# Performance work log

Measured on AMD Instinct MI355X. Metric: run time of the kernel, lower is better.

Reference implementation:

```python
import math
import jax, jax.numpy as jnp
import numpy as np

EPS = 1e-5
NUM_HEADER = 2


def pos_encoding(C, T, dtype):
    i = jnp.arange(C)
    exp = -((i - (i % 2)).astype(dtype) / C)
    freqs = jnp.power(jnp.asarray(10000.0, dtype), exp)[:, None]      # [C,1]
    phases = ((i % 2).astype(dtype) * (np.pi / 2))[:, None]           # [C,1]
    pos = jnp.arange(T, dtype=dtype)[None, :]                         # [1,T]
    return jnp.sin(pos * freqs + phases)                              # [C,T]


def layernorm2d(x, g, b):
    # LayerNorm over (C,T) jointly, per batch element (nn.LayerNorm([C, length]))
    mu = jnp.mean(x, axis=(1, 2), keepdims=True)
    var = jnp.mean((x - mu) ** 2, axis=(1, 2), keepdims=True)
    return (x - mu) * jax.lax.rsqrt(var + EPS) * g[None] + b[None]


def dsconv(x, dw_w, dw_b, pw_w, pw_b):
    # depthwise conv1d (groups=C, 'same' padding for odd k) + pointwise 1x1
    C = x.shape[1]
    k = dw_w.shape[-1]
    y = jax.lax.conv_general_dilated(
        x, dw_w[:, None, :], (1,), [(k // 2, k // 2)],
        dimension_numbers=('NCH', 'OIH', 'NCH'), feature_group_count=C)
    y = y + dw_b[None, :, None]
    y = jnp.einsum('bct,oc->bot', y, pw_w) + pw_b[None, :, None]
    return y


def attention(x, mask, Wq, Wk, Wv, Wo):
    # Faithful to source bug: all heads use Wqs[1]/Wks[1]/Wvs[1] -> identical heads.
    xt = jnp.transpose(x, (0, 2, 1))          # [B,T,C]
    C = xt.shape[-1]
    dk = C / NUM_HEADER
    q = xt @ Wq                               # [B,T,dk]
    k_ = xt @ Wk
    v = xt @ Wv
    s = jnp.einsum('bqd,bkd->bqk', q, k_) * (1.0 / math.sqrt(dk))
    hmask = mask[:, None, :]                  # mask over keys
    s = s * hmask + (1 - hmask) * (-1e30)
    a = jax.nn.softmax(s, axis=2) * mask[:, :, None]
    head = a @ v                              # [B,T,dk]
    heads = jnp.tile(head, (1, 1, NUM_HEADER))  # concat of identical heads
    out = heads @ Wo                          # [B,T,C]
    return jnp.transpose(out, (0, 2, 1))      # [B,C,T]


def setup_inputs() -> dict:
    key = jax.random.key(0)
    B, C, T = 16, 128, 1024
    NCONV, K = 4, 7
    dk = C // NUM_HEADER
    ks = jax.random.split(key, 12)
    inp = {
        'x': jax.random.normal(ks[0], (B, C, T), jnp.float32),
        'mask': jnp.ones((B, T), jnp.float32),
        'dw_w': jax.random.normal(ks[1], (NCONV, C, K), jnp.float32) * math.sqrt(2.0 / K),
        'dw_b': jnp.zeros((NCONV, C), jnp.float32),
        'pw_w': jax.random.normal(ks[2], (NCONV, C, C), jnp.float32) * math.sqrt(2.0 / C),
        'pw_b': jnp.zeros((NCONV, C), jnp.float32),
        'norm0_g': jnp.ones((C, T), jnp.float32),
        'norm0_b': jnp.zeros((C, T), jnp.float32),
        'norms_g': jnp.ones((NCONV, C, T), jnp.float32),
        'norms_b': jnp.zeros((NCONV, C, T), jnp.float32),
        'norme_g': jnp.ones((C, T), jnp.float32),
        'norme_b': jnp.zeros((C, T), jnp.float32),
        'Wq': jax.random.normal(ks[3], (C, dk), jnp.float32) * math.sqrt(2.0 / (C + dk)),
        'Wk': jax.random.normal(ks[4], (C, dk), jnp.float32) * math.sqrt(2.0 / (C + dk)),
        'Wv': jax.random.normal(ks[5], (C, dk), jnp.float32) * math.sqrt(2.0 / (C + dk)),
        'Wo': jax.random.normal(ks[6], (C, C), jnp.float32) * math.sqrt(2.0 / C),
        'fc_w': jax.random.normal(ks[7], (C, C), jnp.float32) * (0.1 * math.sqrt(6.0 / (2 * C))),
        'fc_b': jnp.zeros((C,), jnp.float32),
    }
    return inp


def reference(x, mask, dw_w, dw_b, pw_w, pw_b, norm0_g, norm0_b,
              norms_g, norms_b, norme_g, norme_b,
              Wq, Wk, Wv, Wo, fc_w, fc_b):
    B, C, T = x.shape
    nconv = dw_w.shape[0]
    # dropout is identity in eval mode (reference is deterministic)
    out = x + pos_encoding(C, T, x.dtype)[None]
    res = layernorm2d(out, norm0_g, norm0_b)
    for i in range(nconv):
        out = dsconv(out, dw_w[i], dw_b[i], pw_w[i], pw_b[i])
        out = jax.nn.relu(out)
        out = out + res
        res = out
        out = layernorm2d(out, norms_g[i], norms_b[i])
    out = attention(out, mask, Wq, Wk, Wv, Wo)
    out = out + res
    res = out
    out = layernorm2d(out, norme_g, norme_b)
    out = jnp.einsum('bct,oc->bot', out, fc_w) + fc_b[None, :, None]
    out = jax.nn.relu(out)
    out = out + res
    return out
```

## Files before the change

### kernel.cpp

```cpp
#include <hip/hip_runtime.h>
#include <math.h>

#define BB 16
#define CC 128
#define TT 1024
#define KK 7
#define DK 64
#define NSPLIT 4

typedef float f32x4 __attribute__((ext_vector_type(4)));
typedef short s16x8 __attribute__((ext_vector_type(8)));

__device__ inline short f2bf(float f) {
  union { float f; unsigned u; } v; v.f = f;
  unsigned r = (v.u + 0x7FFFu + ((v.u >> 16) & 1u)) >> 16;
  return (short)r;
}

__device__ inline float bf2f(short s) {
  union { unsigned u; float f; } v;
  v.u = ((unsigned)(unsigned short)s) << 16;
  return v.f;
}

__device__ inline void block_partial_256(float s, float ss, float* dst) {
#pragma unroll
  for (int off = 32; off; off >>= 1) { s += __shfl_xor(s, off); ss += __shfl_xor(ss, off); }
  __shared__ float red[8];
  int w = threadIdx.x >> 6;
  if ((threadIdx.x & 63) == 0) { red[2 * w] = s; red[2 * w + 1] = ss; }
  __syncthreads();
  if (threadIdx.x == 0) {
    for (int i = 1; i < 4; ++i) { s += red[2 * i]; ss += red[2 * i + 1]; }
    dst[0] = s; dst[1] = ss;
  }
}

__device__ inline void ln_stats_from_parts(const float* part_batch, int n, float* sh) {
  if (threadIdx.x < 64) {
    float s = 0.f, ss = 0.f;
    for (int i = threadIdx.x; i < n; i += 64) { s += part_batch[2 * i]; ss += part_batch[2 * i + 1]; }
#pragma unroll
    for (int off = 32; off; off >>= 1) { s += __shfl_xor(s, off); ss += __shfl_xor(ss, off); }
    if (threadIdx.x == 0) {
      const float invN = 1.f / (float)(CC * TT);
      float mu = s * invN;
      sh[0] = mu;
      sh[1] = rsqrtf(ss * invN - mu * mu + 1e-5f);
    }
  }
  __syncthreads();
}

__global__ __launch_bounds__(256) void k_prep0(const float* __restrict__ pww,
                                               const float* __restrict__ Wq,
                                               const float* __restrict__ Wk,
                                               const float* __restrict__ Wv,
                                               const float* __restrict__ Wo,
                                               const float* __restrict__ fcw,
                                               const float* __restrict__ x,
                                               short* __restrict__ pwwb,
                                               short* __restrict__ wqkvb,
                                               short* __restrict__ wo2b,
                                               short* __restrict__ fcwb,
                                               float* __restrict__ part0) {
  if (blockIdx.x < 448) {
    int i = blockIdx.x * 256 + threadIdx.x;
    if (i < 65536) { pwwb[i] = f2bf(pww[i]); return; }
    i -= 65536;
    if (i < 24576) {
      int m = i >> 7, c = i & 127;
      int sel = m >> 6, d = m & 63;
      const float* srcp = sel == 0 ? Wq : (sel == 1 ? Wk : Wv);
      wqkvb[i] = f2bf(srcp[c * DK + d]);
      return;
    }
    i -= 24576;
    if (i < 8192) {
      int o = i >> 6, d = i & 63;
      wo2b[i] = f2bf(Wo[d * CC + o] + Wo[(d + 64) * CC + o]);
      return;
    }
    i -= 8192;
    fcwb[i] = f2bf(fcw[i]);
    return;
  }
  int w = threadIdx.x >> 6, lane = threadIdx.x & 63;
  int bc = (blockIdx.x - 448) * 4 + w;
  int c = bc & (CC - 1);
  float freq = expf(-((float)(c & ~1) * (1.f / (float)CC)) * 9.210340371976184f);
  float ph = (c & 1) ? 1.5707963267948966f : 0.f;
  const float* xr = x + (size_t)bc * TT;
  float s = 0.f, ss = 0.f;
#pragma unroll
  for (int k = 0; k < 4; ++k) {
    int t = (k * 64 + lane) * 4;
    float4 v = *(const float4*)(xr + t);
    v.x += sinf((float)(t + 0) * freq + ph);
    v.y += sinf((float)(t + 1) * freq + ph);
    v.z += sinf((float)(t + 2) * freq + ph);
    v.w += sinf((float)(t + 3) * freq + ph);
    s += v.x + v.y + v.z + v.w;
    ss += v.x * v.x + v.y * v.y + v.z * v.z + v.w * v.w;
  }
#pragma unroll
  for (int off = 32; off; off >>= 1) { s += __shfl_xor(s, off); ss += __shfl_xor(ss, off); }
  if (lane == 0) { part0[(size_t)bc * 2] = s; part0[(size_t)bc * 2 + 1] = ss; }
}

template <bool LN_IN, bool LN_RES, bool ADD_POS>
__global__ __launch_bounds__(256) void k_dsconv(const float* __restrict__ in,
                                                const float* __restrict__ lng,
                                                const float* __restrict__ lnb,
                                                const float* __restrict__ part_in, int npart,
                                                const float* __restrict__ dww,
                                                const float* __restrict__ dwb,
                                                const short* __restrict__ pwwb,
                                                const float* __restrict__ pwb,
                                                float* __restrict__ out,
                                                float* __restrict__ part_out) {
  int tile = blockIdx.x & 31, b = blockIdx.x >> 5;
  int t0 = tile * 32;
  __shared__ float stats[2];
  __shared__ float xs[CC][41];
  __shared__ float xr2[CC][33];
  __shared__ __align__(16) short Dt[32][136];
  ln_stats_from_parts(part_in + (size_t)b * npart * 2, npart, stats);
  float mu = stats[0], rs = stats[1];

  for (int i = threadIdx.x; i < CC * 10; i += 256) {
    int c = i / 10, q = i - c * 10;
    int tb = t0 - 4 + q * 4;
    const float* rowp = in + ((size_t)b * CC + c) * TT;
    float freq = 0.f, ph = 0.f;
    if (ADD_POS) {
      freq = expf(-((float)(c & ~1) * (1.f / (float)CC)) * 9.210340371976184f);
      ph = (c & 1) ? 1.5707963267948966f : 0.f;
    }
    float r0, r1, r2, r3, o0, o1, o2, o3;
    bool full = (tb >= 0) && (tb + 4 <= TT);
    if (full) {
      float4 v = *(const float4*)(rowp + tb);
      if (ADD_POS) {
        v.x += sinf((float)(tb + 0) * freq + ph);
        v.y += sinf((float)(tb + 1) * freq + ph);
        v.z += sinf((float)(tb + 2) * freq + ph);
        v.w += sinf((float)(tb + 3) * freq + ph);
      }
      r0 = v.x; r1 = v.y; r2 = v.z; r3 = v.w;
      o0 = r0; o1 = r1; o2 = r2; o3 = r3;
      if (LN_IN) {
        float4 g = *(const float4*)(lng + (size_t)c * TT + tb);
        float4 bv = *(const float4*)(lnb + (size_t)c * TT + tb);
        o0 = (r0 - mu) * rs * g.x + bv.x;
        o1 = (r1 - mu) * rs * g.y + bv.y;
        o2 = (r2 - mu) * rs * g.z + bv.z;
        o3 = (r3 - mu) * rs * g.w + bv.w;
      }
    } else {
      float rr[4], oo[4];
#pragma unroll
      for (int k = 0; k < 4; ++k) {
        int t = tb + k;
        bool inb = (t >= 0) && (t < TT);
        float rv = 0.f;
        if (inb) {
          rv = rowp[t];
          if (ADD_POS) rv += sinf((float)t * freq + ph);
        }
        rr[k] = rv;
        float ov = rv;
        if (LN_IN && inb)
          ov = (rv - mu) * rs * lng[(size_t)c * TT + t] + lnb[(size_t)c * TT + t];
        oo[k] = ov;
      }
      r0 = rr[0]; r1 = rr[1]; r2 = rr[2]; r3 = rr[3];
      o0 = oo[0]; o1 = oo[1]; o2 = oo[2]; o3 = oo[3];
    }
    if (LN_IN && q >= 1 && q <= 8) {
      int tl = (q - 1) * 4;
      xr2[c][tl] = r0; xr2[c][tl + 1] = r1; xr2[c][tl + 2] = r2; xr2[c][tl + 3] = r3;
    }
    int base = q * 4;
    xs[c][base] = o0; xs[c][base + 1] = o1; xs[c][base + 2] = o2; xs[c][base + 3] = o3;
  }
  __syncthreads();
  for (int i = threadIdx.x; i < 32 * CC; i += 256) {
    int t = i >> 7, c = i & 127;
    float a = dwb[c];
#pragma unroll
    for (int j = 0; j < KK; ++j) a += dww[c * KK + j] * xs[c][t + j + 1];
    Dt[t][c] = f2bf(a);
  }
  __syncthreads();

  int w = threadIdx.x >> 6, lane = threadIdx.x & 63;
  int lo = lane & 15, hi = lane >> 4;
  f32x4 acc[2][2];
#pragma unroll
  for (int mt = 0; mt < 2; ++mt)
#pragma unroll
    for (int nt = 0; nt < 2; ++nt) { acc[mt][nt][0] = 0.f; acc[mt][nt][1] = 0.f; acc[mt][nt][2] = 0.f; acc[mt][nt][3] = 0.f; }
#pragma unroll
  for (int ks = 0; ks < 4; ++ks) {
    s16x8 b0 = *(const s16x8*)&Dt[lo][ks * 32 + hi * 8];
    s16x8 b1 = *(const s16x8*)&Dt[16 + lo][ks * 32 + hi * 8];
    s16x8 a0 = *(const s16x8*)&pwwb[(size_t)(w * 32 + lo) * CC + ks * 32 + hi * 8];
    s16x8 a1 = *(const s16x8*)&pwwb[(size_t)(w * 32 + 16 + lo) * CC + ks * 32 + hi * 8];
    acc[0][0] = __builtin_amdgcn_mfma_f32_16x16x32_bf16(a0, b0, acc[0][0], 0, 0, 0);
    acc[0][1] = __builtin_amdgcn_mfma_f32_16x16x32_bf16(a0, b1, acc[0][1], 0, 0, 0);
    acc[1][0] = __builtin_amdgcn_mfma_f32_16x16x32_bf16(a1, b0, acc[1][0], 0, 0, 0);
    acc[1][1] = __builtin_amdgcn_mfma_f32_16x16x32_bf16(a1, b1, acc[1][1], 0, 0, 0);
  }

  float s = 0.f, ss = 0.f;
#pragma unroll
  for (int mt = 0; mt < 2; ++mt)
#pragma unroll
    for (int nt = 0; nt < 2; ++nt)
#pragma unroll
      for (int r = 0; r < 4; ++r) {
        int row = w * 32 + mt * 16 + hi * 4 + r;
        int tl = nt * 16 + lo;
        int t = t0 + tl;
        float v = acc[mt][nt][r] + pwb[row];
        v = v > 0.f ? v : 0.f;
        float rv;
        if (LN_RES) {
          float raw = xs[row][tl + 4];
          rv = (raw - mu) * rs * lng[row * TT + t] + lnb[row * TT + t];
        } else if (LN_IN) {
          rv = xr2[row][tl];
        } else {
          rv = xs[row][tl + 4];
        }
        v += rv;
        xr2[row][tl] = v;
        s += v; ss += v * v;
      }
  __syncthreads();
  for (int u = threadIdx.x; u < 1024; u += 256) {
    int c = u >> 3, q = u & 7;
    float4 o4;
    o4.x = xr2[c][q * 4]; o4.y = xr2[c][q * 4 + 1];
    o4.z = xr2[c][q * 4 + 2]; o4.w = xr2[c][q * 4 + 3];
    *(float4*)(out + ((size_t)b * CC + c) * TT + t0 + q * 4) = o4;
  }
  block_partial_256(s, ss, part_out + (size_t)blockIdx.x * 2);
}

__global__ __launch_bounds__(256) void k_qkv(const float* __restrict__ in,
                                             const float* __restrict__ lng,
                                             const float* __restrict__ lnb,
                                             const float* __restrict__ part_in,
                                             const short* __restrict__ wqkvb,
                                             short* __restrict__ q,
                                             short* __restrict__ k,
                                             short* __restrict__ vt) {
  int tile = blockIdx.x & 31, b = blockIdx.x >> 5;
  int t0 = tile * 32;
  __shared__ float stats[2];
  __shared__ __align__(16) short Dt[32][136];
  __shared__ __align__(16) short stgQ[32 * 64];
  __shared__ __align__(16) short stgK[32 * 64];
  __shared__ __align__(16) short stgV[64][40];
  ln_stats_from_parts(part_in + (size_t)b * 64, 32, stats);
  float mu = stats[0], rs = stats[1];
  for (int i = threadIdx.x; i < CC * 8; i += 256) {
    int c = i >> 3, qq = i & 7;
    int t = qq * 4;
    size_t off = (size_t)c * TT + t0 + t;
    float4 v = *(const float4*)(in + (size_t)b * CC * TT + off);
    float4 g = *(const float4*)(lng + off);
    float4 bb = *(const float4*)(lnb + off);
    Dt[t + 0][c] = f2bf((v.x - mu) * rs * g.x + bb.x);
    Dt[t + 1][c] = f2bf((v.y - mu) * rs * g.y + bb.y);
    Dt[t + 2][c] = f2bf((v.z - mu) * rs * g.z + bb.z);
    Dt[t + 3][c] = f2bf((v.w - mu) * rs * g.w + bb.w);
  }
  __syncthreads();

  int w = threadIdx.x >> 6, lane = threadIdx.x & 63;
  int lo = lane & 15, hi = lane >> 4;
  f32x4 acc[3][2];
#pragma unroll
  for (int mt = 0; mt < 3; ++mt)
#pragma unroll
    for (int nt = 0; nt < 2; ++nt) { acc[mt][nt][0] = 0.f; acc[mt][nt][1] = 0.f; acc[mt][nt][2] = 0.f; acc[mt][nt][3] = 0.f; }
#pragma unroll
  for (int ks = 0; ks < 4; ++ks) {
    s16x8 b0 = *(const s16x8*)&Dt[lo][ks * 32 + hi * 8];
    s16x8 b1 = *(const s16x8*)&Dt[16 + lo][ks * 32 + hi * 8];
#pragma unroll
    for (int mt = 0; mt < 3; ++mt) {
      s16x8 a = *(const s16x8*)&wqkvb[(size_t)(w * 48 + mt * 16 + lo) * CC + ks * 32 + hi * 8];
      acc[mt][0] = __builtin_amdgcn_mfma_f32_16x16x32_bf16(a, b0, acc[mt][0], 0, 0, 0);
      acc[mt][1] = __builtin_amdgcn_mfma_f32_16x16x32_bf16(a, b1, acc[mt][1], 0, 0, 0);
    }
  }
#pragma unroll
  for (int mt = 0; mt < 3; ++mt)
#pragma unroll
    for (int nt = 0; nt < 2; ++nt) {
      int m0 = w * 48 + mt * 16 + hi * 4;
      int tl = nt * 16 + lo;
      short pv[4];
#pragma unroll
      for (int j = 0; j < 4; ++j) pv[j] = f2bf(acc[mt][nt][j]);
      if (m0 < 64) {
        *(short4*)&stgQ[tl * 64 + m0] = make_short4(pv[0], pv[1], pv[2], pv[3]);
      } else if (m0 < 128) {
        *(short4*)&stgK[tl * 64 + (m0 - 64)] = make_short4(pv[0], pv[1], pv[2], pv[3]);
      } else {
        int d = m0 - 128;
#pragma unroll
        for (int j = 0; j < 4; ++j) stgV[d + j][tl] = pv[j];
      }
    }
  __syncthreads();
  {
    int t = threadIdx.x >> 3, ch = threadIdx.x & 7;
    *(s16x8*)(q + ((size_t)b * TT + t0 + t) * DK + ch * 8) = *(const s16x8*)&stgQ[t * 64 + ch * 8];
    *(s16x8*)(k + ((size_t)b * TT + t0 + t) * DK + ch * 8) = *(const s16x8*)&stgK[t * 64 + ch * 8];
    int d = threadIdx.x >> 2, cv = threadIdx.x & 3;
    *(s16x8*)(vt + ((size_t)b * DK + d) * TT + t0 + cv * 8) = *(const s16x8*)&stgV[d][cv * 8];
  }
}

__global__ __launch_bounds__(128) void k_attn(const short* __restrict__ qb,
                                              const short* __restrict__ kbuf,
                                              const short* __restrict__ vtb,
                                              const float* __restrict__ mask,
                                              short* __restrict__ pacch,
                                              float* __restrict__ pml) {
  int sp = blockIdx.x & (NSPLIT - 1);
  int qt = (blockIdx.x >> 2) & 31;
  int b = blockIdx.x >> 7;
  int w = threadIdx.x >> 6, lane = threadIdx.x & 63;
  int lo = lane & 15, hi = lane >> 4;

  __shared__ __align__(16) short ks[64][72];
  __shared__ __align__(16) short vt[64][72];
  __shared__ __align__(16) short ps[2][16][68];
  __shared__ float ms[64];

  const short* qp = qb + ((size_t)b * TT + qt * 32 + w * 16 + lo) * DK + hi * 8;
  s16x8 aq0 = *(const s16x8*)qp;
  s16x8 aq1 = *(const s16x8*)(qp + 32);

  f32x4 acc[4];
  float m_i[4], l_i[4];
#pragma unroll
  for (int r = 0; r < 4; ++r) {
    m_i[r] = -3.0e38f; l_i[r] = 0.f;
#pragma unroll
    for (int nt = 0; nt < 4; ++nt) acc[nt][r] = 0.f;
  }
  const float scale = 0.125f;

  for (int kb2 = sp * (TT / 64 / NSPLIT); kb2 < (sp + 1) * (TT / 64 / NSPLIT); ++kb2) {
    __syncthreads();
    for (int i = threadIdx.x; i < 512; i += 128) {
      int r = i >> 3, ch = i & 7;
      *(s16x8*)&ks[r][ch * 8] =
          *(const s16x8*)(kbuf + ((size_t)b * TT + kb2 * 64 + r) * DK + ch * 8);
      *(s16x8*)&vt[r][ch * 8] =
          *(const s16x8*)(vtb + ((size_t)b * DK + r) * TT + kb2 * 64 + ch * 8);
    }
    if (threadIdx.x < 64) ms[threadIdx.x] = mask[(size_t)b * TT + kb2 * 64 + threadIdx.x];
    __syncthreads();

    f32x4 sc[4];
#pragma unroll
    for (int nt = 0; nt < 4; ++nt) {
      f32x4 z; z[0] = 0.f; z[1] = 0.f; z[2] = 0.f; z[3] = 0.f;
      s16x8 bk0 = *(const s16x8*)&ks[nt * 16 + lo][hi * 8];
      s16x8 bk1 = *(const s16x8*)&ks[nt * 16 + lo][32 + hi * 8];
      z = __builtin_amdgcn_mfma_f32_16x16x32_bf16(aq0, bk0, z, 0, 0, 0);
      z = __builtin_amdgcn_mfma_f32_16x16x32_bf16(aq1, bk1, z, 0, 0, 0);
      sc[nt] = z;
    }
#pragma unroll
    for (int nt = 0; nt < 4; ++nt) {
      float mv = ms[nt * 16 + lo];
      float addv = (1.f - mv) * -1e30f;
#pragma unroll
      for (int r = 0; r < 4; ++r) sc[nt][r] = sc[nt][r] * scale * mv + addv;
    }
    float alpha[4];
#pragma unroll
    for (int r = 0; r < 4; ++r) {
      float m0 = fmaxf(fmaxf(sc[0][r], sc[1][r]), fmaxf(sc[2][r], sc[3][r]));
#pragma unroll
      for (int off = 1; off < 16; off <<= 1) m0 = fmaxf(m0, __shfl_xor(m0, off));
      float mn = fmaxf(m_i[r], m0);
      alpha[r] = __expf(m_i[r] - mn);
      m_i[r] = mn;
    }
    float psum[4] = {0.f, 0.f, 0.f, 0.f};
#pragma unroll
    for (int nt = 0; nt < 4; ++nt)
#pragma unroll
      for (int r = 0; r < 4; ++r) {
        float p = __expf(sc[nt][r] - m_i[r]);
        psum[r] += p;
        ps[w][hi * 4 + r][nt * 16 + lo] = f2bf(p);
      }
#pragma unroll
    for (int r = 0; r < 4; ++r) {
      float sum = psum[r];
#pragma unroll
      for (int off = 1; off < 16; off <<= 1) sum += __shfl_xor(sum, off);
      l_i[r] = l_i[r] * alpha[r] + sum;
    }
#pragma unroll
    for (int nt = 0; nt < 4; ++nt)
#pragma unroll
      for (int r = 0; r < 4; ++r) acc[nt][r] *= alpha[r];

    s16x8 ap0 = *(const s16x8*)&ps[w][lo][hi * 8];
    s16x8 ap1 = *(const s16x8*)&ps[w][lo][32 + hi * 8];
#pragma unroll
    for (int nt = 0; nt < 4; ++nt) {
      s16x8 bv0 = *(const s16x8*)&vt[nt * 16 + lo][hi * 8];
      s16x8 bv1 = *(const s16x8*)&vt[nt * 16 + lo][32 + hi * 8];
      acc[nt] = __builtin_amdgcn_mfma_f32_16x16x32_bf16(ap0, bv0, acc[nt], 0, 0, 0);
      acc[nt] = __builtin_amdgcn_mfma_f32_16x16x32_bf16(ap1, bv1, acc[nt], 0, 0, 0);
    }
  }
  __syncthreads();
  short* pc = &ks[0][0];
#pragma unroll
  for (int r = 0; r < 4; ++r) {
    int row = w * 16 + hi * 4 + r;
#pragma unroll
    for (int nt = 0; nt < 4; ++nt) pc[row * 64 + nt * 16 + lo] = f2bf(acc[nt][r]);
    if (lo == 0) {
      size_t mb = (((size_t)b * TT + qt * 32 + row) * NSPLIT + sp) * 2;
      pml[mb] = m_i[r];
      pml[mb + 1] = l_i[r];
    }
  }
  __syncthreads();
  for (int u = threadIdx.x; u < 256; u += 128) {
    int row = u >> 3, ch = u & 7;
    size_t pb = (((size_t)b * TT + qt * 32 + row) * NSPLIT + sp) * DK;
    *(s16x8*)(pacch + pb + ch * 8) = *(const s16x8*)&pc[row * 64 + ch * 8];
  }
}

__global__ __launch_bounds__(256) void k_attnout2(const short* __restrict__ pacch,
                                                  const float* __restrict__ pml,
                                                  const float* __restrict__ mask,
                                                  const short* __restrict__ wo2b,
                                                  const float* __restrict__ res,
                                                  float* __restrict__ out,
                                                  float* __restrict__ part_out) {
  int tile = blockIdx.x & 31, b = blockIdx.x >> 5;
  int t0 = tile * 32;
  __shared__ __align__(16) short Ht[32][72];
  __shared__ float ot[128][33];
  {
    int i = threadIdx.x;
    int tr = i >> 3, q = i & 7;
    size_t rb = (size_t)b * TT + t0 + tr;
    float m[NSPLIT], l[NSPLIT];
#pragma unroll
    for (int s = 0; s < NSPLIT; ++s) {
      m[s] = pml[(rb * NSPLIT + s) * 2];
      l[s] = pml[(rb * NSPLIT + s) * 2 + 1];
    }
    float M = fmaxf(fmaxf(m[0], m[1]), fmaxf(m[2], m[3]));
    float wgt[NSPLIT], L = 0.f;
#pragma unroll
    for (int s = 0; s < NSPLIT; ++s) { wgt[s] = __expf(m[s] - M); L += wgt[s] * l[s]; }
    float inv = mask[rb] / L;
    float o[8] = {0.f, 0.f, 0.f, 0.f, 0.f, 0.f, 0.f, 0.f};
#pragma unroll
    for (int s = 0; s < NSPLIT; ++s) {
      s16x8 pv = *(const s16x8*)(pacch + (rb * NSPLIT + s) * DK + q * 8);
#pragma unroll
      for (int j = 0; j < 8; ++j) o[j] += wgt[s] * bf2f(pv[j]);
    }
    short h[8];
#pragma unroll
    for (int j = 0; j < 8; ++j) h[j] = f2bf(o[j] * inv);
    *(s16x8*)&Ht[tr][q * 8] = *(const s16x8*)h;
  }
  __syncthreads();

  int w = threadIdx.x >> 6, lane = threadIdx.x & 63;
  int lo = lane & 15, hi = lane >> 4;
  f32x4 acc[2][2];
#pragma unroll
  for (int mt = 0; mt < 2; ++mt)
#pragma unroll
    for (int nt = 0; nt < 2; ++nt) { acc[mt][nt][0] = 0.f; acc[mt][nt][1] = 0.f; acc[mt][nt][2] = 0.f; acc[mt][nt][3] = 0.f; }
#pragma unroll
  for (int ks = 0; ks < 2; ++ks) {
    s16x8 b0 = *(const s16x8*)&Ht[lo][ks * 32 + hi * 8];
    s16x8 b1 = *(const s16x8*)&Ht[16 + lo][ks * 32 + hi * 8];
    s16x8 a0 = *(const s16x8*)&wo2b[(size_t)(w * 32 + lo) * DK + ks * 32 + hi * 8];
    s16x8 a1 = *(const s16x8*)&wo2b[(size_t)(w * 32 + 16 + lo) * DK + ks * 32 + hi * 8];
    acc[0][0] = __builtin_amdgcn_mfma_f32_16x16x32_bf16(a0, b0, acc[0][0], 0, 0, 0);
    acc[0][1] = __builtin_amdgcn_mfma_f32_16x16x32_bf16(a0, b1, acc[0][1], 0, 0, 0);
    acc[1][0] = __builtin_amdgcn_mfma_f32_16x16x32_bf16(a1, b0, acc[1][0], 0, 0, 0);
    acc[1][1] = __builtin_amdgcn_mfma_f32_16x16x32_bf16(a1, b1, acc[1][1], 0, 0, 0);
  }
  float s = 0.f, ss = 0.f;
#pragma unroll
  for (int mt = 0; mt < 2; ++mt)
#pragma unroll
    for (int nt = 0; nt < 2; ++nt)
#pragma unroll
      for (int r = 0; r < 4; ++r) {
        int row = w * 32 + mt * 16 + hi * 4 + r;
        int tl = nt * 16 + lo;
        size_t idx = ((size_t)b * CC + row) * TT + t0 + tl;
        float v = acc[mt][nt][r] + res[idx];
        ot[row][tl] = v;
        s += v; ss += v * v;
      }
  __syncthreads();
  for (int u = threadIdx.x; u < 1024; u += 256) {
    int c = u >> 3, q = u & 7;
    float4 o4;
    o4.x = ot[c][q * 4]; o4.y = ot[c][q * 4 + 1];
    o4.z = ot[c][q * 4 + 2]; o4.w = ot[c][q * 4 + 3];
    *(float4*)(out + ((size_t)b * CC + c) * TT + t0 + q * 4) = o4;
  }
  block_partial_256(s, ss, part_out + (size_t)blockIdx.x * 2);
}

__global__ __launch_bounds__(256) void k_fc(const float* __restrict__ in,
                                            const float* __restrict__ lng,
                                            const float* __restrict__ lnb,
                                            const float* __restrict__ part_in,
                                            const short* __restrict__ fcwb,
                                            const float* __restrict__ fb,
                                            float* __restrict__ out) {
  int tile = blockIdx.x & 31, b = blockIdx.x >> 5;
  int t0 = tile * 32;
  __shared__ float stats[2];
  __shared__ float xr2[CC][33];
  __shared__ __align__(16) short Dt[32][136];
  ln_stats_from_parts(part_in + (size_t)b * 64, 32, stats);
  float mu = stats[0], rs = stats[1];
  for (int i = threadIdx.x; i < CC * 8; i += 256) {
    int c = i >> 3, q = i & 7;
    int t = q * 4;
    size_t off = (size_t)c * TT + t0 + t;
    float4 v = *(const float4*)(in + (size_t)b * CC * TT + off);
    float4 g = *(const float4*)(lng + off);
    float4 bb = *(const float4*)(lnb + off);
    xr2[c][t] = v.x; xr2[c][t + 1] = v.y; xr2[c][t + 2] = v.z; xr2[c][t + 3] = v.w;
    Dt[t + 0][c] = f2bf((v.x - mu) * rs * g.x + bb.x);
    Dt[t + 1][c] = f2bf((v.y - mu) * rs * g.y + bb.y);
    Dt[t + 2][c] = f2bf((v.z - mu) * rs * g.z + bb.z);
    Dt[t + 3][c] = f2bf((v.w - mu) * rs * g.w + bb.w);
  }
  __syncthreads();

  int w = threadIdx.x >> 6, lane = threadIdx.x & 63;
  int lo = lane & 15, hi = lane >> 4;
  f32x4 acc[2][2];
#pragma unroll
  for (int mt = 0; mt < 2; ++mt)
#pragma unroll
    for (int nt = 0; nt < 2; ++nt) { acc[mt][nt][0] = 0.f; acc[mt][nt][1] = 0.f; acc[mt][nt][2] = 0.f; acc[mt][nt][3] = 0.f; }
#pragma unroll
  for (int ks = 0; ks < 4; ++ks) {
    s16x8 b0 = *(const s16x8*)&Dt[lo][ks * 32 + hi * 8];
    s16x8 b1 = *(const s16x8*)&Dt[16 + lo][ks * 32 + hi * 8];
    s16x8 a0 = *(const s16x8*)&fcwb[(size_t)(w * 32 + lo) * CC + ks * 32 + hi * 8];
    s16x8 a1 = *(const s16x8*)&fcwb[(size_t)(w * 32 + 16 + lo) * CC + ks * 32 + hi * 8];
    acc[0][0] = __builtin_amdgcn_mfma_f32_16x16x32_bf16(a0, b0, acc[0][0], 0, 0, 0);
    acc[0][1] = __builtin_amdgcn_mfma_f32_16x16x32_bf16(a0, b1, acc[0][1], 0, 0, 0);
    acc[1][0] = __builtin_amdgcn_mfma_f32_16x16x32_bf16(a1, b0, acc[1][0], 0, 0, 0);
    acc[1][1] = __builtin_amdgcn_mfma_f32_16x16x32_bf16(a1, b1, acc[1][1], 0, 0, 0);
  }
#pragma unroll
  for (int mt = 0; mt < 2; ++mt)
#pragma unroll
    for (int nt = 0; nt < 2; ++nt)
#pragma unroll
      for (int r = 0; r < 4; ++r) {
        int row = w * 32 + mt * 16 + hi * 4 + r;
        int tl = nt * 16 + lo;
        float v = acc[mt][nt][r] + fb[row];
        v = v > 0.f ? v : 0.f;
        xr2[row][tl] = v + xr2[row][tl];
      }
  __syncthreads();
  for (int u = threadIdx.x; u < 1024; u += 256) {
    int c = u >> 3, q = u & 7;
    float4 o4;
    o4.x = xr2[c][q * 4]; o4.y = xr2[c][q * 4 + 1];
    o4.z = xr2[c][q * 4 + 2]; o4.w = xr2[c][q * 4 + 3];
    *(float4*)(out + ((size_t)b * CC + c) * TT + t0 + q * 4) = o4;
  }
}

extern "C" void kernel_launch(void* const* d_in, const int* in_sizes, int n_in,
                              void* d_out, int out_size, void* d_ws, size_t ws_size,
                              hipStream_t stream) {
  const float* x    = (const float*)d_in[0];
  const float* mask = (const float*)d_in[1];
  const float* dww  = (const float*)d_in[2];
  const float* dwb  = (const float*)d_in[3];
  const float* pww  = (const float*)d_in[4];
  const float* pwb  = (const float*)d_in[5];
  const float* n0g  = (const float*)d_in[6];
  const float* n0b  = (const float*)d_in[7];
  const float* nsg  = (const float*)d_in[8];
  const float* nsb  = (const float*)d_in[9];
  const float* neg_ = (const float*)d_in[10];
  const float* neb  = (const float*)d_in[11];
  const float* Wq   = (const float*)d_in[12];
  const float* Wk   = (const float*)d_in[13];
  const float* Wv   = (const float*)d_in[14];
  const float* Wo   = (const float*)d_in[15];
  const float* fcw  = (const float*)d_in[16];
  const float* fcb  = (const float*)d_in[17];
  float* out = (float*)d_out;

  float* W = (float*)d_ws;
  const size_t NBCT = (size_t)BB * CC * TT;
  const size_t NBTD = (size_t)BB * TT * DK;
  const size_t CT = (size_t)CC * TT;
  float* O     = W;
  float* S     = W + NBCT;
  float* PART0 = W + 2 * NBCT;
  float* PARTS = PART0 + 4096;
  float* PML   = PARTS + 5 * 1024;
  short* QB    = (short*)(PML + (size_t)BB * TT * NSPLIT * 2);
  short* KB    = QB + NBTD;
  short* VT    = KB + NBTD;
  short* PACCH = VT + NBTD;
  short* PWWB  = PACCH + NBTD * NSPLIT;
  short* WQKVB = PWWB + 65536;
  short* WO2B  = WQKVB + 24576;
  short* FCWB  = WO2B + 8192;

  k_prep0<<<960, 256, 0, stream>>>(pww, Wq, Wk, Wv, Wo, fcw, x,
                                   PWWB, WQKVB, WO2B, FCWB, PART0);
  k_dsconv<false, true, true><<<BB * 32, 256, 0, stream>>>(
      x, n0g, n0b, PART0, 128, dww, dwb, PWWB, pwb, S, PARTS);
  k_dsconv<true, false, false><<<BB * 32, 256, 0, stream>>>(
      S, nsg + 0 * CT, nsb + 0 * CT, PARTS, 32,
      dww + 1 * CC * KK, dwb + 1 * CC, PWWB + 1 * CC * CC, pwb + 1 * CC, O, PARTS + 1024);
  k_dsconv<true, false, false><<<BB * 32, 256, 0, stream>>>(
      O, nsg + 1 * CT, nsb + 1 * CT, PARTS + 1024, 32,
      dww + 2 * CC * KK, dwb + 2 * CC, PWWB + 2 * CC * CC, pwb + 2 * CC, S, PARTS + 2048);
  k_dsconv<true, false, false><<<BB * 32, 256, 0, stream>>>(
      S, nsg + 2 * CT, nsb + 2 * CT, PARTS + 2048, 32,
      dww + 3 * CC * KK, dwb + 3 * CC, PWWB + 3 * CC * CC, pwb + 3 * CC, O, PARTS + 3072);
  k_qkv<<<BB * 32, 256, 0, stream>>>(O, nsg + 3 * CT, nsb + 3 * CT, PARTS + 3072,
                                     WQKVB, QB, KB, VT);
  k_attn<<<BB * 32 * NSPLIT, 128, 0, stream>>>(QB, KB, VT, mask, PACCH, PML);
  k_attnout2<<<BB * 32, 256, 0, stream>>>(PACCH, PML, mask, WO2B, O, S, PARTS + 4096);
  k_fc<<<BB * 32, 256, 0, stream>>>(S, neg_, neb, PARTS + 4096, FCWB, fcb, out);
}
```

Baseline: 192.7 us.

## Fuse split-K flash attention with output projection in one kernel

Merges the split-K attention kernel and the combine/output-projection kernel into one 256-thread kernel. Each block handles a 32-query tile, and its two 128-thread halves process the two halves of the keys. They then combine their partial softmax state through shared memory before running the Wo projection, residual add and LN partial sums. This removes the global round trip of bf16 partial accumulators and m/l values and one kernel launch. In exchange the attention grid shrinks from 2048 to 512 blocks, and each half walks 8 key blocks serially instead of 4, which reduces parallelism.

```diff
diff --git a/kernel.cpp b/kernel.cpp
--- a/kernel.cpp
+++ b/kernel.cpp
@@ -6,7 +6,6 @@
 #define TT 1024
 #define KK 7
 #define DK 64
-#define NSPLIT 4
 
 typedef float f32x4 __attribute__((ext_vector_type(4)));
 typedef short s16x8 __attribute__((ext_vector_type(8)));
@@ -15,12 +14,6 @@
   union { float f; unsigned u; } v; v.f = f;
   unsigned r = (v.u + 0x7FFFu + ((v.u >> 16) & 1u)) >> 16;
   return (short)r;
-}
-
-__device__ inline float bf2f(short s) {
-  union { unsigned u; float f; } v;
-  v.u = ((unsigned)(unsigned short)s) << 16;
-  return v.f;
 }
 
 __device__ inline void block_partial_256(float s, float ss, float* dst) {
@@ -327,24 +320,39 @@
   }
 }
 
-__global__ __launch_bounds__(128) void k_attn(const short* __restrict__ qb,
-                                              const short* __restrict__ kbuf,
-                                              const short* __restrict__ vtb,
-                                              const float* __restrict__ mask,
-                                              short* __restrict__ pacch,
-                                              float* __restrict__ pml) {
-  int sp = blockIdx.x & (NSPLIT - 1);
-  int qt = (blockIdx.x >> 2) & 31;
-  int b = blockIdx.x >> 7;
-  int w = threadIdx.x >> 6, lane = threadIdx.x & 63;
-  int lo = lane & 15, hi = lane >> 4;
-
-  __shared__ __align__(16) short ks[64][72];
-  __shared__ __align__(16) short vt[64][72];
-  __shared__ __align__(16) short ps[2][16][68];
-  __shared__ float ms[64];
-
-  const short* qp = qb + ((size_t)b * TT + qt * 32 + w * 16 + lo) * DK + hi * 8;
+struct AtHalf {
+  short ks[64][72];
+  short vt[64][72];
+  short ps[2][16][68];
+  float ms[64];
+};
+union AtShared {
+  AtHalf h[2];
+  float ot[128 * 33];
+};
+
+__global__ __launch_bounds__(256) void k_attnfused(const short* __restrict__ qb,
+                                                   const short* __restrict__ kbuf,
+                                                   const short* __restrict__ vtb,
+                                                   const float* __restrict__ mask,
+                                                   const short* __restrict__ wo2b,
+                                                   const float* __restrict__ res,
+                                                   float* __restrict__ out,
+                                                   float* __restrict__ part_out) {
+  int tile = blockIdx.x & 31, b = blockIdx.x >> 5;
+  int t0 = tile * 32;
+  __shared__ AtShared U;
+  __shared__ __align__(16) short Ht[32][72];
+
+  const int tid = threadIdx.x;
+  const int half = tid >> 7;
+  const int ltid = tid & 127;
+  const int hw = ltid >> 6;
+  const int lane = ltid & 63;
+  const int lo = lane & 15, hi = lane >> 4;
+  AtHalf& A = U.h[half];
+
+  const short* qp = qb + ((size_t)b * TT + t0 + hw * 16 + lo) * DK + hi * 8;
   s16x8 aq0 = *(const s16x8*)qp;
   s16x8 aq1 = *(const s16x8*)(qp + 32);
 
@@ -358,31 +366,32 @@
   }
   const float scale = 0.125f;
 
-  for (int kb2 = sp * (TT / 64 / NSPLIT); kb2 < (sp + 1) * (TT / 64 / NSPLIT); ++kb2) {
+  for (int it2 = 0; it2 < 8; ++it2) {
+    int kb2 = half * 8 + it2;
     __syncthreads();
-    for (int i = threadIdx.x; i < 512; i += 128) {
+    for (int i = ltid; i < 512; i += 128) {
       int r = i >> 3, ch = i & 7;
-      *(s16x8*)&ks[r][ch * 8] =
+      *(s16x8*)&A.ks[r][ch * 8] =
           *(const s16x8*)(kbuf + ((size_t)b * TT + kb2 * 64 + r) * DK + ch * 8);
-      *(s16x8*)&vt[r][ch * 8] =
+      *(s16x8*)&A.vt[r][ch * 8] =
           *(const s16x8*)(vtb + ((size_t)b * DK + r) * TT + kb2 * 64 + ch * 8);
     }
-    if (threadIdx.x < 64) ms[threadIdx.x] = mask[(size_t)b * TT + kb2 * 64 + threadIdx.x];
+    if (ltid < 64) A.ms[ltid] = mask[(size_t)b * TT + kb2 * 64 + ltid];
     __syncthreads();
 
     f32x4 sc[4];
 #pragma unroll
     for (int nt = 0; nt < 4; ++nt) {
       f32x4 z; z[0] = 0.f; z[1] = 0.f; z[2] = 0.f; z[3] = 0.f;
-      s16x8 bk0 = *(const s16x8*)&ks[nt * 16 + lo][hi * 8];
-      s16x8 bk1 = *(const s16x8*)&ks[nt * 16 + lo][32 + hi * 8];
+      s16x8 bk0 = *(const s16x8*)&A.ks[nt * 16 + lo][hi * 8];
+      s16x8 bk1 = *(const s16x8*)&A.ks[nt * 16 + lo][32 + hi * 8];
       z = __builtin_amdgcn_mfma_f32_16x16x32_bf16(aq0, bk0, z, 0, 0, 0);
       z = __builtin_amdgcn_mfma_f32_16x16x32_bf16(aq1, bk1, z, 0, 0, 0);
       sc[nt] = z;
     }
 #pragma unroll
     for (int nt = 0; nt < 4; ++nt) {
-      float mv = ms[nt * 16 + lo];
+      float mv = A.ms[nt * 16 + lo];
       float addv = (1.f - mv) * -1e30f;
 #pragma unroll
       for (int r = 0; r < 4; ++r) sc[nt][r] = sc[nt][r] * scale * mv + addv;
@@ -404,7 +413,7 @@
       for (int r = 0; r < 4; ++r) {
         float p = __expf(sc[nt][r] - m_i[r]);
         psum[r] += p;
-        ps[w][hi * 4 + r][nt * 16 + lo] = f2bf(p);
+        A.ps[hw][hi * 4 + r][nt * 16 + lo] = f2bf(p);
       }
 #pragma unroll
     for (int r = 0; r < 4; ++r) {
@@ -418,95 +427,66 @@
 #pragma unroll
       for (int r = 0; r < 4; ++r) acc[nt][r] *= alpha[r];
 
-    s16x8 ap0 = *(const s16x8*)&ps[w][lo][hi * 8];
-    s16x8 ap1 = *(const s16x8*)&ps[w][lo][32 + hi * 8];
+    s16x8 ap0 = *(const s16x8*)&A.ps[hw][lo][hi * 8];
+    s16x8 ap1 = *(const s16x8*)&A.ps[hw][lo][32 + hi * 8];
 #pragma unroll
     for (int nt = 0; nt < 4; ++nt) {
-      s16x8 bv0 = *(const s16x8*)&vt[nt * 16 + lo][hi * 8];
-      s16x8 bv1 = *(const s16x8*)&vt[nt * 16 + lo][32 + hi * 8];
+      s16x8 bv0 = *(const s16x8*)&A.vt[nt * 16 + lo][hi * 8];
+      s16x8 bv1 = *(const s16x8*)&A.vt[nt * 16 + lo][32 + hi * 8];
       acc[nt] = __builtin_amdgcn_mfma_f32_16x16x32_bf16(ap0, bv0, acc[nt], 0, 0, 0);
       acc[nt] = __builtin_amdgcn_mfma_f32_16x16x32_bf16(ap1, bv1, acc[nt], 0, 0, 0);
     }
   }
   __syncthreads();
-  short* pc = &ks[0][0];
-#pragma unroll
-  for (int r = 0; r < 4; ++r) {
-    int row = w * 16 + hi * 4 + r;
-#pragma unroll
-    for (int nt = 0; nt < 4; ++nt) pc[row * 64 + nt * 16 + lo] = f2bf(acc[nt][r]);
-    if (lo == 0) {
-      size_t mb = (((size_t)b * TT + qt * 32 + row) * NSPLIT + sp) * 2;
-      pml[mb] = m_i[r];
-      pml[mb + 1] = l_i[r];
-    }
-  }
-  __syncthreads();
-  for (int u = threadIdx.x; u < 256; u += 128) {
-    int row = u >> 3, ch = u & 7;
-    size_t pb = (((size_t)b * TT + qt * 32 + row) * NSPLIT + sp) * DK;
-    *(s16x8*)(pacch + pb + ch * 8) = *(const s16x8*)&pc[row * 64 + ch * 8];
-  }
-}
-
-__global__ __launch_bounds__(256) void k_attnout2(const short* __restrict__ pacch,
-                                                  const float* __restrict__ pml,
-                                                  const float* __restrict__ mask,
-                                                  const short* __restrict__ wo2b,
-                                                  const float* __restrict__ res,
-                                                  float* __restrict__ out,
-                                                  float* __restrict__ part_out) {
-  int tile = blockIdx.x & 31, b = blockIdx.x >> 5;
-  int t0 = tile * 32;
-  __shared__ __align__(16) short Ht[32][72];
-  __shared__ float ot[128][33];
-  {
-    int i = threadIdx.x;
-    int tr = i >> 3, q = i & 7;
-    size_t rb = (size_t)b * TT + t0 + tr;
-    float m[NSPLIT], l[NSPLIT];
-#pragma unroll
-    for (int s = 0; s < NSPLIT; ++s) {
-      m[s] = pml[(rb * NSPLIT + s) * 2];
-      l[s] = pml[(rb * NSPLIT + s) * 2 + 1];
-    }
-    float M = fmaxf(fmaxf(m[0], m[1]), fmaxf(m[2], m[3]));
-    float wgt[NSPLIT], L = 0.f;
-#pragma unroll
-    for (int s = 0; s < NSPLIT; ++s) { wgt[s] = __expf(m[s] - M); L += wgt[s] * l[s]; }
-    float inv = mask[rb] / L;
-    float o[8] = {0.f, 0.f, 0.f, 0.f, 0.f, 0.f, 0.f, 0.f};
-#pragma unroll
-    for (int s = 0; s < NSPLIT; ++s) {
-      s16x8 pv = *(const s16x8*)(pacch + (rb * NSPLIT + s) * DK + q * 8);
-#pragma unroll
-      for (int j = 0; j < 8; ++j) o[j] += wgt[s] * bf2f(pv[j]);
-    }
-    short h[8];
-#pragma unroll
-    for (int j = 0; j < 8; ++j) h[j] = f2bf(o[j] * inv);
-    *(s16x8*)&Ht[tr][q * 8] = *(const s16x8*)h;
-  }
-  __syncthreads();
-
-  int w = threadIdx.x >> 6, lane = threadIdx.x & 63;
-  int lo = lane & 15, hi = lane >> 4;
-  f32x4 acc[2][2];
+  float* cmb = (float*)&U.h[0];
+  float* ml1 = (float*)&U.h[1];
+  if (half == 1) {
+#pragma unroll
+    for (int r = 0; r < 4; ++r) {
+      int row = hw * 16 + hi * 4 + r;
+#pragma unroll
+      for (int nt = 0; nt < 4; ++nt) cmb[row * 64 + nt * 16 + lo] = acc[nt][r];
+      if (lo == 0) { ml1[row * 2] = m_i[r]; ml1[row * 2 + 1] = l_i[r]; }
+    }
+  }
+  __syncthreads();
+  if (half == 0) {
+#pragma unroll
+    for (int r = 0; r < 4; ++r) {
+      int row = hw * 16 + hi * 4 + r;
+      float m1 = ml1[row * 2], l1 = ml1[row * 2 + 1];
+      float M = fmaxf(m_i[r], m1);
+      float w0 = __expf(m_i[r] - M), w1 = __expf(m1 - M);
+      float L = w0 * l_i[r] + w1 * l1;
+      float inv = mask[(size_t)b * TT + t0 + row] / L;
+#pragma unroll
+      for (int nt = 0; nt < 4; ++nt)
+        Ht[row][nt * 16 + lo] =
+            f2bf((w0 * acc[nt][r] + w1 * cmb[row * 64 + nt * 16 + lo]) * inv);
+    }
+  }
+  __syncthreads();
+  int w4 = tid >> 6;
+  int flane = tid & 63;
+  int flo = flane & 15, fhi = flane >> 4;
+  f32x4 acc2[2][2];
 #pragma unroll
   for (int mt = 0; mt < 2; ++mt)
 #pragma unroll
-    for (int nt = 0; nt < 2; ++nt) { acc[mt][nt][0] = 0.f; acc[mt][nt][1] = 0.f; acc[mt][nt][2] = 0.f; acc[mt][nt][3] = 0.f; }
+    for (int nt = 0; nt < 2; ++nt) { acc2[mt][nt][0] = 0.f; acc2[mt][nt][1] = 0.f; acc2[mt][nt][2] = 0.f; acc2[mt][nt][3] = 0.f; }
 #pragma unroll
   for (int ks = 0; ks < 2; ++ks) {
-    s16x8 b0 = *(const s16x8*)&Ht[lo][ks * 32 + hi * 8];
-    s16x8 b1 = *(const s16x8*)&Ht[16 + lo][ks * 32 + hi * 8];
-    s16x8 a0 = *(const s16x8*)&wo2b[(size_t)(w * 32 + lo) * DK + ks * 32 + hi * 8];
-    s16x8 a1 = *(const s16x8*)&wo2b[(size_t)(w * 32 + 16 + lo) * DK + ks * 32 + hi * 8];
-    acc[0][0] = __builtin_amdgcn_mfma_f32_16x16x32_bf16(a0, b0, acc[0][0], 0, 0, 0);
-    acc[0][1] = __builtin_amdgcn_mfma_f32_16x16x32_bf16(a0, b1, acc[0][1], 0, 0, 0);
-    acc[1][0] = __builtin_amdgcn_mfma_f32_16x16x32_bf16(a1, b0, acc[1][0], 0, 0, 0);
-    acc[1][1] = __builtin_amdgcn_mfma_f32_16x16x32_bf16(a1, b1, acc[1][1], 0, 0, 0);
-  }
+    s16x8 b0 = *(const s16x8*)&Ht[flo][ks * 32 + fhi * 8];
+    s16x8 b1 = *(const s16x8*)&Ht[16 + flo][ks * 32 + fhi * 8];
+    s16x8 a0 = *(const s16x8*)&wo2b[(size_t)(w4 * 32 + flo) * DK + ks * 32 + fhi * 8];
+    s16x8 a1 = *(const s16x8*)&wo2b[(size_t)(w4 * 32 + 16 + flo) * DK + ks * 32 + fhi * 8];
+    acc2[0][0] = __builtin_amdgcn_mfma_f32_16x16x32_bf16(a0, b0, acc2[0][0], 0, 0, 0);
+    acc2[0][1] = __builtin_amdgcn_mfma_f32_16x16x32_bf16(a0, b1, acc2[0][1], 0, 0, 0);
+    acc2[1][0] = __builtin_amdgcn_mfma_f32_16x16x32_bf16(a1, b0, acc2[1][0], 0, 0, 0);
+    acc2[1][1] = __builtin_amdgcn_mfma_f32_16x16x32_bf16(a1, b1, acc2[1][1], 0, 0, 0);
+  }
+  __syncthreads();
+  float* otp = U.ot;
   float s = 0.f, ss = 0.f;
 #pragma unroll
   for (int mt = 0; mt < 2; ++mt)
@@ -514,19 +494,19 @@
     for (int nt = 0; nt < 2; ++nt)
 #pragma unroll
       for (int r = 0; r < 4; ++r) {
-        int row = w * 32 + mt * 16 + hi * 4 + r;
-        int tl = nt * 16 + lo;
+        int row = w4 * 32 + mt * 16 + fhi * 4 + r;
+        int tl = nt * 16 + flo;
         size_t idx = ((size_t)b * CC + row) * TT + t0 + tl;
-        float v = acc[mt][nt][r] + res[idx];
-        ot[row][tl] = v;
+        float v = acc2[mt][nt][r] + res[idx];
+        otp[row * 33 + tl] = v;
         s += v; ss += v * v;
       }
   __syncthreads();
-  for (int u = threadIdx.x; u < 1024; u += 256) {
+  for (int u = tid; u < 1024; u += 256) {
     int c = u >> 3, q = u & 7;
     float4 o4;
-    o4.x = ot[c][q * 4]; o4.y = ot[c][q * 4 + 1];
-    o4.z = ot[c][q * 4 + 2]; o4.w = ot[c][q * 4 + 3];
+    o4.x = otp[c * 33 + q * 4]; o4.y = otp[c * 33 + q * 4 + 1];
+    o4.z = otp[c * 33 + q * 4 + 2]; o4.w = otp[c * 33 + q * 4 + 3];
     *(float4*)(out + ((size_t)b * CC + c) * TT + t0 + q * 4) = o4;
   }
   block_partial_256(s, ss, part_out + (size_t)blockIdx.x * 2);
@@ -632,12 +612,10 @@
   float* S     = W + NBCT;
   float* PART0 = W + 2 * NBCT;
   float* PARTS = PART0 + 4096;
-  float* PML   = PARTS + 5 * 1024;
-  short* QB    = (short*)(PML + (size_t)BB * TT * NSPLIT * 2);
+  short* QB    = (short*)(PARTS + 5 * 1024);
   short* KB    = QB + NBTD;
   short* VT    = KB + NBTD;
-  short* PACCH = VT + NBTD;
-  short* PWWB  = PACCH + NBTD * NSPLIT;
+  short* PWWB  = VT + NBTD;
   short* WQKVB = PWWB + 65536;
   short* WO2B  = WQKVB + 24576;
   short* FCWB  = WO2B + 8192;
@@ -657,7 +635,6 @@
       dww + 3 * CC * KK, dwb + 3 * CC, PWWB + 3 * CC * CC, pwb + 3 * CC, O, PARTS + 3072);
   k_qkv<<<BB * 32, 256, 0, stream>>>(O, nsg + 3 * CT, nsb + 3 * CT, PARTS + 3072,
                                      WQKVB, QB, KB, VT);
-  k_attn<<<BB * 32 * NSPLIT, 128, 0, stream>>>(QB, KB, VT, mask, PACCH, PML);
-  k_attnout2<<<BB * 32, 256, 0, stream>>>(PACCH, PML, mask, WO2B, O, S, PARTS + 4096);
+  k_attnfused<<<BB * 32, 256, 0, stream>>>(QB, KB, VT, mask, WO2B, O, S, PARTS + 4096);
   k_fc<<<BB * 32, 256, 0, stream>>>(S, neg_, neb, PARTS + 4096, FCWB, fcb, out);
 }
```

Measured after the change: 200.6 us. +4.1%, slower.

## Prefetch tile inputs before LN stats reduction and register-double-buffer attention K/V

Applied to the files above, without the earlier changes.

In the dsconv, qkv and fc kernels, all global loads of activations and LN gamma/beta are issued into registers before the LayerNorm statistics reduction. The normalization is applied only after that reduction, so load latency overlaps the stats barrier. The flash-attention split kernel now prefetches the next K/V block into registers while the current block is computed, and the combine kernel hoists its partial-accumulator loads. The cost is higher register pressure, which may lower occupancy.

```diff
diff --git a/kernel.cpp b/kernel.cpp
--- a/kernel.cpp
+++ b/kernel.cpp
@@ -125,10 +125,12 @@
   __shared__ float xs[CC][41];
   __shared__ float xr2[CC][33];
   __shared__ __align__(16) short Dt[32][136];
-  ln_stats_from_parts(part_in + (size_t)b * npart * 2, npart, stats);
-  float mu = stats[0], rs = stats[1];
-
-  for (int i = threadIdx.x; i < CC * 10; i += 256) {
+
+  float rx[5][4];
+  float gx[LN_IN ? 5 : 1][4], bx[LN_IN ? 5 : 1][4];
+#pragma unroll
+  for (int k5 = 0; k5 < 5; ++k5) {
+    int i = threadIdx.x + k5 * 256;
     int c = i / 10, q = i - c * 10;
     int tb = t0 - 4 + q * 4;
     const float* rowp = in + ((size_t)b * CC + c) * TT;
@@ -137,7 +139,6 @@
       freq = expf(-((float)(c & ~1) * (1.f / (float)CC)) * 9.210340371976184f);
       ph = (c & 1) ? 1.5707963267948966f : 0.f;
     }
-    float r0, r1, r2, r3, o0, o1, o2, o3;
     bool full = (tb >= 0) && (tb + 4 <= TT);
     if (full) {
       float4 v = *(const float4*)(rowp + tb);
@@ -147,42 +148,50 @@
         v.z += sinf((float)(tb + 2) * freq + ph);
         v.w += sinf((float)(tb + 3) * freq + ph);
       }
-      r0 = v.x; r1 = v.y; r2 = v.z; r3 = v.w;
-      o0 = r0; o1 = r1; o2 = r2; o3 = r3;
+      rx[k5][0] = v.x; rx[k5][1] = v.y; rx[k5][2] = v.z; rx[k5][3] = v.w;
       if (LN_IN) {
         float4 g = *(const float4*)(lng + (size_t)c * TT + tb);
         float4 bv = *(const float4*)(lnb + (size_t)c * TT + tb);
-        o0 = (r0 - mu) * rs * g.x + bv.x;
-        o1 = (r1 - mu) * rs * g.y + bv.y;
-        o2 = (r2 - mu) * rs * g.z + bv.z;
-        o3 = (r3 - mu) * rs * g.w + bv.w;
+        gx[k5][0] = g.x; gx[k5][1] = g.y; gx[k5][2] = g.z; gx[k5][3] = g.w;
+        bx[k5][0] = bv.x; bx[k5][1] = bv.y; bx[k5][2] = bv.z; bx[k5][3] = bv.w;
       }
     } else {
-      float rr[4], oo[4];
-#pragma unroll
-      for (int k = 0; k < 4; ++k) {
-        int t = tb + k;
+#pragma unroll
+      for (int kk = 0; kk < 4; ++kk) {
+        int t = tb + kk;
         bool inb = (t >= 0) && (t < TT);
         float rv = 0.f;
         if (inb) {
           rv = rowp[t];
           if (ADD_POS) rv += sinf((float)t * freq + ph);
         }
-        rr[k] = rv;
-        float ov = rv;
-        if (LN_IN && inb)
-          ov = (rv - mu) * rs * lng[(size_t)c * TT + t] + lnb[(size_t)c * TT + t];
-        oo[k] = ov;
-      }
-      r0 = rr[0]; r1 = rr[1]; r2 = rr[2]; r3 = rr[3];
-      o0 = oo[0]; o1 = oo[1]; o2 = oo[2]; o3 = oo[3];
+        rx[k5][kk] = rv;
+        if (LN_IN) {
+          gx[k5][kk] = inb ? lng[(size_t)c * TT + t] : 0.f;
+          bx[k5][kk] = inb ? lnb[(size_t)c * TT + t] : 0.f;
+        }
+      }
+    }
+  }
+  ln_stats_from_parts(part_in + (size_t)b * npart * 2, npart, stats);
+  float mu = stats[0], rs = stats[1];
+#pragma unroll
+  for (int k5 = 0; k5 < 5; ++k5) {
+    int i = threadIdx.x + k5 * 256;
+    int c = i / 10, q = i - c * 10;
+    int base = q * 4;
+#pragma unroll
+    for (int kk = 0; kk < 4; ++kk) {
+      float rv = rx[k5][kk];
+      float ov = rv;
+      if (LN_IN) ov = (rv - mu) * rs * gx[k5][kk] + bx[k5][kk];
+      xs[c][base + kk] = ov;
     }
     if (LN_IN && q >= 1 && q <= 8) {
       int tl = (q - 1) * 4;
-      xr2[c][tl] = r0; xr2[c][tl + 1] = r1; xr2[c][tl + 2] = r2; xr2[c][tl + 3] = r3;
-    }
-    int base = q * 4;
-    xs[c][base] = o0; xs[c][base + 1] = o1; xs[c][base + 2] = o2; xs[c][base + 3] = o3;
+#pragma unroll
+      for (int kk = 0; kk < 4; ++kk) xr2[c][tl + kk] = rx[k5][kk];
+    }
   }
   __syncthreads();
   for (int i = threadIdx.x; i < 32 * CC; i += 256) {
@@ -264,19 +273,30 @@
   __shared__ __align__(16) short stgQ[32 * 64];
   __shared__ __align__(16) short stgK[32 * 64];
   __shared__ __align__(16) short stgV[64][40];
-  ln_stats_from_parts(part_in + (size_t)b * 64, 32, stats);
-  float mu = stats[0], rs = stats[1];
-  for (int i = threadIdx.x; i < CC * 8; i += 256) {
+  float rxq[4][4], gxq[4][4], bxq[4][4];
+#pragma unroll
+  for (int k4 = 0; k4 < 4; ++k4) {
+    int i = threadIdx.x + k4 * 256;
     int c = i >> 3, qq = i & 7;
     int t = qq * 4;
     size_t off = (size_t)c * TT + t0 + t;
     float4 v = *(const float4*)(in + (size_t)b * CC * TT + off);
     float4 g = *(const float4*)(lng + off);
     float4 bb = *(const float4*)(lnb + off);
-    Dt[t + 0][c] = f2bf((v.x - mu) * rs * g.x + bb.x);
-    Dt[t + 1][c] = f2bf((v.y - mu) * rs * g.y + bb.y);
-    Dt[t + 2][c] = f2bf((v.z - mu) * rs * g.z + bb.z);
-    Dt[t + 3][c] = f2bf((v.w - mu) * rs * g.w + bb.w);
+    rxq[k4][0] = v.x; rxq[k4][1] = v.y; rxq[k4][2] = v.z; rxq[k4][3] = v.w;
+    gxq[k4][0] = g.x; gxq[k4][1] = g.y; gxq[k4][2] = g.z; gxq[k4][3] = g.w;
+    bxq[k4][0] = bb.x; bxq[k4][1] = bb.y; bxq[k4][2] = bb.z; bxq[k4][3] = bb.w;
+  }
+  ln_stats_from_parts(part_in + (size_t)b * 64, 32, stats);
+  float mu = stats[0], rs = stats[1];
+#pragma unroll
+  for (int k4 = 0; k4 < 4; ++k4) {
+    int i = threadIdx.x + k4 * 256;
+    int c = i >> 3, qq = i & 7;
+    int t = qq * 4;
+#pragma unroll
+    for (int kk = 0; kk < 4; ++kk)
+      Dt[t + kk][c] = f2bf((rxq[k4][kk] - mu) * rs * gxq[k4][kk] + bxq[k4][kk]);
   }
   __syncthreads();
 
@@ -357,18 +377,38 @@
     for (int nt = 0; nt < 4; ++nt) acc[nt][r] = 0.f;
   }
   const float scale = 0.125f;
-
-  for (int kb2 = sp * (TT / 64 / NSPLIT); kb2 < (sp + 1) * (TT / 64 / NSPLIT); ++kb2) {
+  const int kb0 = sp * (TT / 64 / NSPLIT);
+
+  s16x8 kreg[4], vreg[4];
+#pragma unroll
+  for (int j = 0; j < 4; ++j) {
+    int i = threadIdx.x + j * 128;
+    int r = i >> 3, ch = i & 7;
+    kreg[j] = *(const s16x8*)(kbuf + ((size_t)b * TT + kb0 * 64 + r) * DK + ch * 8);
+    vreg[j] = *(const s16x8*)(vtb + ((size_t)b * DK + r) * TT + kb0 * 64 + ch * 8);
+  }
+
+  for (int it = 0; it < 4; ++it) {
+    int kb2 = kb0 + it;
     __syncthreads();
-    for (int i = threadIdx.x; i < 512; i += 128) {
+#pragma unroll
+    for (int j = 0; j < 4; ++j) {
+      int i = threadIdx.x + j * 128;
       int r = i >> 3, ch = i & 7;
-      *(s16x8*)&ks[r][ch * 8] =
-          *(const s16x8*)(kbuf + ((size_t)b * TT + kb2 * 64 + r) * DK + ch * 8);
-      *(s16x8*)&vt[r][ch * 8] =
-          *(const s16x8*)(vtb + ((size_t)b * DK + r) * TT + kb2 * 64 + ch * 8);
+      *(s16x8*)&ks[r][ch * 8] = kreg[j];
+      *(s16x8*)&vt[r][ch * 8] = vreg[j];
     }
     if (threadIdx.x < 64) ms[threadIdx.x] = mask[(size_t)b * TT + kb2 * 64 + threadIdx.x];
     __syncthreads();
+    if (it < 3) {
+#pragma unroll
+      for (int j = 0; j < 4; ++j) {
+        int i = threadIdx.x + j * 128;
+        int r = i >> 3, ch = i & 7;
+        kreg[j] = *(const s16x8*)(kbuf + ((size_t)b * TT + (kb2 + 1) * 64 + r) * DK + ch * 8);
+        vreg[j] = *(const s16x8*)(vtb + ((size_t)b * DK + r) * TT + (kb2 + 1) * 64 + ch * 8);
+      }
+    }
 
     f32x4 sc[4];
 #pragma unroll
@@ -464,6 +504,10 @@
     int i = threadIdx.x;
     int tr = i >> 3, q = i & 7;
     size_t rb = (size_t)b * TT + t0 + tr;
+    s16x8 pvv[NSPLIT];
+#pragma unroll
+    for (int s = 0; s < NSPLIT; ++s)
+      pvv[s] = *(const s16x8*)(pacch + (rb * NSPLIT + s) * DK + q * 8);
     float m[NSPLIT], l[NSPLIT];
 #pragma unroll
     for (int s = 0; s < NSPLIT; ++s) {
@@ -478,9 +522,8 @@
     float o[8] = {0.f, 0.f, 0.f, 0.f, 0.f, 0.f, 0.f, 0.f};
 #pragma unroll
     for (int s = 0; s < NSPLIT; ++s) {
-      s16x8 pv = *(const s16x8*)(pacch + (rb * NSPLIT + s) * DK + q * 8);
-#pragma unroll
-      for (int j = 0; j < 8; ++j) o[j] += wgt[s] * bf2f(pv[j]);
+#pragma unroll
+      for (int j = 0; j < 8; ++j) o[j] += wgt[s] * bf2f(pvv[s][j]);
     }
     short h[8];
 #pragma unroll
@@ -544,20 +587,32 @@
   __shared__ float stats[2];
   __shared__ float xr2[CC][33];
   __shared__ __align__(16) short Dt[32][136];
-  ln_stats_from_parts(part_in + (size_t)b * 64, 32, stats);
-  float mu = stats[0], rs = stats[1];
-  for (int i = threadIdx.x; i < CC * 8; i += 256) {
+  float rxq[4][4], gxq[4][4], bxq[4][4];
+#pragma unroll
+  for (int k4 = 0; k4 < 4; ++k4) {
+    int i = threadIdx.x + k4 * 256;
     int c = i >> 3, q = i & 7;
     int t = q * 4;
     size_t off = (size_t)c * TT + t0 + t;
     float4 v = *(const float4*)(in + (size_t)b * CC * TT + off);
     float4 g = *(const float4*)(lng + off);
     float4 bb = *(const float4*)(lnb + off);
-    xr2[c][t] = v.x; xr2[c][t + 1] = v.y; xr2[c][t + 2] = v.z; xr2[c][t + 3] = v.w;
-    Dt[t + 0][c] = f2bf((v.x - mu) * rs * g.x + bb.x);
-    Dt[t + 1][c] = f2bf((v.y - mu) * rs * g.y + bb.y);
-    Dt[t + 2][c] = f2bf((v.z - mu) * rs * g.z + bb.z);
-    Dt[t + 3][c] = f2bf((v.w - mu) * rs * g.w + bb.w);
+    rxq[k4][0] = v.x; rxq[k4][1] = v.y; rxq[k4][2] = v.z; rxq[k4][3] = v.w;
+    gxq[k4][0] = g.x; gxq[k4][1] = g.y; gxq[k4][2] = g.z; gxq[k4][3] = g.w;
+    bxq[k4][0] = bb.x; bxq[k4][1] = bb.y; bxq[k4][2] = bb.z; bxq[k4][3] = bb.w;
+  }
+  ln_stats_from_parts(part_in + (size_t)b * 64, 32, stats);
+  float mu = stats[0], rs = stats[1];
+#pragma unroll
+  for (int k4 = 0; k4 < 4; ++k4) {
+    int i = threadIdx.x + k4 * 256;
+    int c = i >> 3, q = i & 7;
+    int t = q * 4;
+#pragma unroll
+    for (int kk = 0; kk < 4; ++kk) {
+      xr2[c][t + kk] = rxq[k4][kk];
+      Dt[t + kk][c] = f2bf((rxq[k4][kk] - mu) * rs * gxq[k4][kk] + bxq[k4][kk]);
+    }
   }
   __syncthreads();
 
```

Result: no change. 193.7 us (+0.5%).
